# Kernel tuning notes

Measured on AMD Instinct MI355X. Metric: run time of the kernel, lower is better.

The kernel has to match this reference:

```python
import jax, jax.numpy as jnp
import numpy as np

N = 50000
E = 600000
D_IN = 128
D_HID = 128
D_OUT = 40
BN_EPS = 1e-5


def setup_inputs() -> dict:
    key = jax.random.key(0)
    ks = jax.random.split(key, 16)
    g = lambda k, *s: (jax.random.normal(k, s, jnp.float32) * 0.05)
    return {
        "x": jax.random.normal(ks[0], (N, D_IN), jnp.float32),
        "edge_index": jax.random.randint(ks[1], (2, E), 0, N, dtype=jnp.int64),
        "W0": g(ks[2], D_IN, D_HID), "b0": jnp.zeros((D_HID,), jnp.float32),
        "W1": g(ks[3], D_HID, D_HID), "b1": jnp.zeros((D_HID,), jnp.float32),
        "W2": g(ks[4], D_HID, D_OUT), "b2": jnp.zeros((D_OUT,), jnp.float32),
        "g0": 1.0 + g(ks[5], D_HID), "be0": g(ks[6], D_HID),
        "m0": g(ks[7], D_HID), "v0": 0.5 + jax.random.uniform(ks[8], (D_HID,), jnp.float32),
        "g1": 1.0 + g(ks[9], D_HID), "be1": g(ks[10], D_HID),
        "m1": g(ks[11], D_HID), "v1": 0.5 + jax.random.uniform(ks[12], (D_HID,), jnp.float32),
    }


def reference(x, edge_index, W0, b0, W1, b1, W2, b2,
              g0, be0, m0, v0, g1, be1, m1, v1):
    n = x.shape[0]
    loop = jnp.arange(n, dtype=edge_index.dtype)
    # GCN with self-loops: A_hat = A + I, symmetric normalization
    src = jnp.concatenate([edge_index[0], loop])
    dst = jnp.concatenate([edge_index[1], loop])
    deg = jax.ops.segment_sum(jnp.ones_like(dst, jnp.float32), dst, num_segments=n)
    dinv = jax.lax.rsqrt(jnp.maximum(deg, 1.0))
    norm = dinv[src] * dinv[dst]  # [E+N]

    def conv(h, W, b):
        h = h @ W + b                                   # [N, d_out]
        msg = norm[:, None] * h[src]                    # gather + scale
        return jax.ops.segment_sum(msg, dst, num_segments=n)

    def bn_relu(h, g, be, m, v):
        return jax.nn.relu((h - m) * (g * jax.lax.rsqrt(v + BN_EPS)) + be)

    h = bn_relu(conv(x, W0, b0), g0, be0, m0, v0)
    h = bn_relu(conv(h, W1, b1), g1, be1, m1, v1)
    h = conv(h, W2, b2)
    return jax.nn.log_softmax(h, axis=-1)
```

## Files before the change

kernel.cpp:

```cpp
#include <hip/hip_runtime.h>
#include <math.h>

#define BN_EPS 1e-5f
#define CAP 96

typedef unsigned short ushort_t;
typedef __attribute__((ext_vector_type(8))) short short8;
typedef __attribute__((ext_vector_type(4))) float floatx4;

__device__ inline ushort_t f2b(float f) {
    unsigned u = __float_as_uint(f);
    unsigned r = u + 0x7FFFu + ((u >> 16) & 1u);
    return (ushort_t)(r >> 16);
}
__device__ inline float b2f(ushort_t b) { return __uint_as_float(((unsigned)b) << 16); }
__device__ inline float2 u2f2(unsigned u) {
    return make_float2(b2f((ushort_t)(u & 0xffffu)), b2f((ushort_t)(u >> 16)));
}

__global__ __launch_bounds__(256) void fill_ell_cast(
    const int* __restrict__ ei, int* __restrict__ cnt, ushort_t* __restrict__ ell,
    const float* __restrict__ W0, const float* __restrict__ W1, const float* __restrict__ W2,
    ushort_t* __restrict__ Wt0, ushort_t* __restrict__ Wt1, ushort_t* __restrict__ Wt2,
    int E, int FB)
{
    int bid = blockIdx.x;
    if (bid < FB) {
        int e = bid * 256 + threadIdx.x;
        if (e < E) {
            int s = ei[e];
            int d = ei[E + e];
            int p = atomicAdd(&cnt[d], 1);
            if (p < CAP) ell[(size_t)d * CAP + p] = (ushort_t)s;
        }
        return;
    }
    int i = (bid - FB) * 256 + threadIdx.x;
    if (i < 16384) {
        int n = i >> 7, k = i & 127;
        Wt0[i] = f2b(W0[k * 128 + n]);
    } else if (i < 32768) {
        int j = i - 16384;
        int n = j >> 7, k = j & 127;
        Wt1[j] = f2b(W1[k * 128 + n]);
    } else if (i < 40960) {
        int j = i - 32768;
        int n = j >> 7, k = j & 127;
        Wt2[j] = (n < 40) ? f2b(W2[k * 40 + n]) : (ushort_t)0;
    }
}

__global__ void make_dinv(const int* __restrict__ cnt, float* __restrict__ dinv, int n) {
    int i = blockIdx.x * blockDim.x + threadIdx.x;
    if (i < n) dinv[i] = rsqrtf((float)(cnt[i] + 1));
}

template<int NT, bool AF32>
__global__ __launch_bounds__(256) void gemm_mfma(const void* __restrict__ Av,
                                                 const ushort_t* __restrict__ Wt,
                                                 const float* __restrict__ bias,
                                                 const float* __restrict__ dinv,
                                                 ushort_t* __restrict__ C,
                                                 int M, int ncols) {
    __shared__ ushort_t Ws[NT * 128];
    const int tid = threadIdx.x;
    const int rbase = blockIdx.x * 128;

#pragma unroll
    for (int p = 0; p < NT / 16; ++p) {
        int cid = p * 256 + tid;
        int nr = cid >> 4, seg = cid & 15;
        *(uint4*)(Ws + nr * 128 + ((seg ^ (nr & 15)) << 3)) =
            *(const uint4*)(Wt + (size_t)cid * 8);
    }
    __syncthreads();

    const int wave = tid >> 6, lane = tid & 63;
    const int m = lane & 15, quad = lane >> 4;
    constexpr int CT = NT / 16;
    floatx4 acc[2][CT];
#pragma unroll
    for (int rt = 0; rt < 2; ++rt)
#pragma unroll
        for (int ct = 0; ct < CT; ++ct) acc[rt][ct] = (floatx4){0.f, 0.f, 0.f, 0.f};

    const int r0 = wave * 32;
    const int ra = rbase + r0 + m;
    const int rb = ra + 16;
    const bool oka = ra < M, okb = rb < M;

#pragma unroll
    for (int ks = 0; ks < 4; ++ks) {
        int ko = ks * 32 + quad * 8;
        short8 a0 = {0, 0, 0, 0, 0, 0, 0, 0}, a1 = a0;
        if (AF32) {
            const float* A32 = (const float*)Av;
            if (oka) {
                const float* p = A32 + (size_t)ra * 128 + ko;
                float4 f0 = *(const float4*)p, f1 = *(const float4*)(p + 4);
                a0[0] = f2b(f0.x); a0[1] = f2b(f0.y); a0[2] = f2b(f0.z); a0[3] = f2b(f0.w);
                a0[4] = f2b(f1.x); a0[5] = f2b(f1.y); a0[6] = f2b(f1.z); a0[7] = f2b(f1.w);
            }
            if (okb) {
                const float* p = A32 + (size_t)rb * 128 + ko;
                float4 f0 = *(const float4*)p, f1 = *(const float4*)(p + 4);
                a1[0] = f2b(f0.x); a1[1] = f2b(f0.y); a1[2] = f2b(f0.z); a1[3] = f2b(f0.w);
                a1[4] = f2b(f1.x); a1[5] = f2b(f1.y); a1[6] = f2b(f1.z); a1[7] = f2b(f1.w);
            }
        } else {
            const ushort_t* A16 = (const ushort_t*)Av;
            if (oka) a0 = *(const short8*)(A16 + (size_t)ra * 128 + ko);
            if (okb) a1 = *(const short8*)(A16 + (size_t)rb * 128 + ko);
        }
#pragma unroll
        for (int ct = 0; ct < CT; ++ct) {
            short8 b = *(const short8*)(Ws + (ct * 16 + m) * 128 + (((ks * 4 + quad) ^ m) << 3));
            acc[0][ct] = __builtin_amdgcn_mfma_f32_16x16x32_bf16(a0, b, acc[0][ct], 0, 0, 0);
            acc[1][ct] = __builtin_amdgcn_mfma_f32_16x16x32_bf16(a1, b, acc[1][ct], 0, 0, 0);
        }
    }

    float dsc[2][4];
#pragma unroll
    for (int rt = 0; rt < 2; ++rt)
#pragma unroll
        for (int r = 0; r < 4; ++r) {
            int gr = rbase + r0 + rt * 16 + quad * 4 + r;
            dsc[rt][r] = (gr < M) ? dinv[gr] : 0.f;
        }

    __syncthreads();
    constexpr int SEGN = NT / 8, CMASK = SEGN - 1;
#pragma unroll
    for (int rt = 0; rt < 2; ++rt)
#pragma unroll
        for (int ct = 0; ct < CT; ++ct) {
            int col = ct * 16 + m;
            float bv = (col < ncols) ? bias[col] : 0.f;
            int seg = col >> 3, cl = col & 7;
#pragma unroll
            for (int r = 0; r < 4; ++r) {
                int row = r0 + rt * 16 + quad * 4 + r;
                Ws[row * NT + ((seg ^ (row & CMASK)) << 3) + cl] =
                    f2b((acc[rt][ct][r] + bv) * dsc[rt][r]);
            }
        }
    __syncthreads();
    constexpr int CPT = (128 * SEGN) / 256;
#pragma unroll
    for (int p = 0; p < CPT; ++p) {
        int cid = p * 256 + tid;
        int row = cid / SEGN, seg = cid & CMASK;
        int gr = rbase + row;
        if (gr < M)
            *(uint4*)(C + (size_t)gr * NT + seg * 8) =
                *(const uint4*)(Ws + row * NT + ((seg ^ (row & CMASK)) << 3));
    }
}

__global__ __launch_bounds__(256) void agg128_bn(const ushort_t* __restrict__ h,
                                                 const int* __restrict__ cnt,
                                                 const ushort_t* __restrict__ ell,
                                                 const float* __restrict__ dinv,
                                                 const float* __restrict__ g,
                                                 const float* __restrict__ be,
                                                 const float* __restrict__ mB,
                                                 const float* __restrict__ v,
                                                 ushort_t* __restrict__ out, int n) {
    int wv = __builtin_amdgcn_readfirstlane((blockIdx.x * 256 + threadIdx.x) >> 6);
    int lane = threadIdx.x & 63;
    if (wv >= n) return;
    const unsigned* h2 = (const unsigned*)h;
    float dv = dinv[wv];
    float2 hv = u2f2(h2[(size_t)wv * 64 + lane]);
    float ax = hv.x, ay = hv.y;
    int c = min(cnt[wv], CAP);
    const ushort_t* row = ell + (size_t)wv * CAP;
    int k = 0;
    for (; k + 8 <= c; k += 8) {
        int s[8];
#pragma unroll
        for (int j = 0; j < 8; ++j) s[j] = row[k + j];
#pragma unroll
        for (int j = 0; j < 8; ++j) {
            float2 t = u2f2(h2[(size_t)s[j] * 64 + lane]);
            ax += t.x;
            ay += t.y;
        }
    }
    if (k < c) {
        int rem = c - k;
        int s[8];
#pragma unroll
        for (int j = 0; j < 8; ++j) {
            int sr = row[k + j];
            s[j] = (j < rem) ? sr : 0;
        }
#pragma unroll
        for (int j = 0; j < 8; ++j) {
            float2 t = u2f2(h2[(size_t)s[j] * 64 + lane]);
            ax += (j < rem) ? t.x : 0.f;
            ay += (j < rem) ? t.y : 0.f;
        }
    }
    ax *= dv;
    ay *= dv;
    int c0 = lane * 2;
    float s0f = g[c0] * rsqrtf(v[c0] + BN_EPS);
    float s1f = g[c0 + 1] * rsqrtf(v[c0 + 1] + BN_EPS);
    float o0 = fmaxf(fmaf(ax - mB[c0], s0f, be[c0]), 0.f);
    float o1 = fmaxf(fmaf(ay - mB[c0 + 1], s1f, be[c0 + 1]), 0.f);
    unsigned ov = (unsigned)f2b(o0) | ((unsigned)f2b(o1) << 16);
    ((unsigned*)out)[(size_t)wv * 64 + lane] = ov;
}

__global__ __launch_bounds__(256) void agg40_lsm(const ushort_t* __restrict__ h,
                                                 const int* __restrict__ cnt,
                                                 const ushort_t* __restrict__ ell,
                                                 const float* __restrict__ dinv,
                                                 float* __restrict__ out, int n) {
    int wv = __builtin_amdgcn_readfirstlane((blockIdx.x * 256 + threadIdx.x) >> 6);
    int lane = threadIdx.x & 63;
    if (wv >= n) return;
    float dv = dinv[wv];
    float acc = b2f(h[(size_t)wv * 64 + lane]);
    int c = min(cnt[wv], CAP);
    const ushort_t* row = ell + (size_t)wv * CAP;
    int k = 0;
    for (; k + 8 <= c; k += 8) {
        int s[8];
#pragma unroll
        for (int j = 0; j < 8; ++j) s[j] = row[k + j];
#pragma unroll
        for (int j = 0; j < 8; ++j) acc += b2f(h[(size_t)s[j] * 64 + lane]);
    }
    if (k < c) {
        int rem = c - k;
        int s[8];
#pragma unroll
        for (int j = 0; j < 8; ++j) {
            int sr = row[k + j];
            s[j] = (j < rem) ? sr : 0;
        }
#pragma unroll
        for (int j = 0; j < 8; ++j) {
            float t = b2f(h[(size_t)s[j] * 64 + lane]);
            acc += (j < rem) ? t : 0.f;
        }
    }
    acc *= dv;
    bool act = lane < 40;
    float x = act ? acc : -INFINITY;
    float mx = x;
#pragma unroll
    for (int off = 32; off > 0; off >>= 1) mx = fmaxf(mx, __shfl_xor(mx, off, 64));
    float ex = act ? expf(acc - mx) : 0.f;
    float se = ex;
#pragma unroll
    for (int off = 32; off > 0; off >>= 1) se += __shfl_xor(se, off, 64);
    float r = acc - mx - logf(se);
    if (act) out[(size_t)wv * 40 + lane] = r;
}


extern "C" void kernel_launch(void* const* d_in, const int* in_sizes, int n_in,
                              void* d_out, int out_size, void* d_ws, size_t ws_size,
                              hipStream_t stream) {
    const float* x = (const float*)d_in[0];
    const int* ei = (const int*)d_in[1];
    const float* W0 = (const float*)d_in[2];
    const float* b0 = (const float*)d_in[3];
    const float* W1 = (const float*)d_in[4];
    const float* b1 = (const float*)d_in[5];
    const float* W2 = (const float*)d_in[6];
    const float* b2 = (const float*)d_in[7];
    const float* g0 = (const float*)d_in[8];
    const float* be0 = (const float*)d_in[9];
    const float* m0 = (const float*)d_in[10];
    const float* v0 = (const float*)d_in[11];
    const float* g1 = (const float*)d_in[12];
    const float* be1 = (const float*)d_in[13];
    const float* m1 = (const float*)d_in[14];
    const float* v1 = (const float*)d_in[15];
    float* out = (float*)d_out;

    const int N = in_sizes[0] / 128;
    const int E = in_sizes[1] / 2;

    char* wp = (char*)d_ws;
    auto alloc = [&](size_t bytes) -> char* {
        char* p = wp;
        wp += (bytes + 255) & ~(size_t)255;
        return p;
    };
    int* cnt = (int*)alloc((size_t)N * 4);
    float* dinv = (float*)alloc((size_t)N * 4);
    ushort_t* ell = (ushort_t*)alloc(((size_t)N * CAP + 16) * 2);
    ushort_t* hA = (ushort_t*)alloc((size_t)N * 128 * 2);
    ushort_t* hB = (ushort_t*)alloc((size_t)N * 128 * 2);
    ushort_t* hA2 = (ushort_t*)alloc((size_t)N * 128 * 2);
    ushort_t* hB2 = (ushort_t*)alloc((size_t)N * 128 * 2);
    ushort_t* hL = (ushort_t*)alloc((size_t)N * 64 * 2);
    ushort_t* Wt0 = (ushort_t*)alloc(128 * 128 * 2);
    ushort_t* Wt1 = (ushort_t*)alloc(128 * 128 * 2);
    ushort_t* Wt2 = (ushort_t*)alloc(64 * 128 * 2);

    const int GB = (N + 127) / 128;
    const int FB = (E + 255) / 256;
    const int CB = 160;

    hipMemsetAsync(cnt, 0, (size_t)N * 4, stream);
    fill_ell_cast<<<FB + CB, 256, 0, stream>>>(ei, cnt, ell, W0, W1, W2,
                                               Wt0, Wt1, Wt2, E, FB);
    make_dinv<<<(N + 255) / 256, 256, 0, stream>>>(cnt, dinv, N);

    gemm_mfma<128, true><<<GB, 256, 0, stream>>>(x, Wt0, b0, dinv, hA, N, 128);
    agg128_bn<<<(N + 3) / 4, 256, 0, stream>>>(hA, cnt, ell, dinv, g0, be0, m0, v0, hB, N);
    gemm_mfma<128, false><<<GB, 256, 0, stream>>>(hB, Wt1, b1, dinv, hA2, N, 128);
    agg128_bn<<<(N + 3) / 4, 256, 0, stream>>>(hA2, cnt, ell, dinv, g1, be1, m1, v1, hB2, N);
    gemm_mfma<64, false><<<GB, 256, 0, stream>>>(hB2, Wt2, b2, dinv, hL, N, 40);
    agg40_lsm<<<(N + 3) / 4, 256, 0, stream>>>(hL, cnt, ell, dinv, out, N);
}
```

Baseline: 231.8 us.

## Fuse all GCN stages into one cooperative persistent kernel with grid syncs

Replaces the sequence of eight launches (memset, fill, dinv, three GEMMs, three aggregations) with a single cooperative kernel. It runs persistent grid-stride loops over each phase and separates them with grid.sync. dinv is recomputed inline from the counts instead of being stored in its own buffer. This is meant to remove launch gaps and tail effects between stages, but it adds the cost of grid-wide barriers and limits each phase to a fixed resident grid, capped at 1024 blocks. The persistent GEMM also reloads the weights into LDS for every tile. A multi-kernel fallback path is kept in case the cooperative launch fails.

New measurement: 680.8 us. +193.7%, slower.

```diff
diff --git a/kernel.cpp b/kernel.cpp
--- a/kernel.cpp
+++ b/kernel.cpp
@@ -1,8 +1,12 @@
 #include <hip/hip_runtime.h>
+#include <hip/hip_cooperative_groups.h>
 #include <math.h>
+
+namespace cg = cooperative_groups;
 
 #define BN_EPS 1e-5f
 #define CAP 96
+#define GRID_MAX 1024
 
 typedef unsigned short ushort_t;
 typedef __attribute__((ext_vector_type(8))) short short8;
@@ -18,7 +22,291 @@
     return make_float2(b2f((ushort_t)(u & 0xffffu)), b2f((ushort_t)(u >> 16)));
 }
 
-__global__ __launch_bounds__(256) void fill_ell_cast(
+template<int NT, bool AF32>
+__device__ void gemm_phase(ushort_t* __restrict__ Ws,
+                           const void* __restrict__ Av,
+                           const ushort_t* __restrict__ Wt,
+                           const float* __restrict__ bias,
+                           const int* __restrict__ cnt,
+                           ushort_t* __restrict__ C,
+                           int M, int ncols) {
+    const int tid = threadIdx.x;
+    const int ntiles = (M + 127) >> 7;
+    const int wave = tid >> 6, lane = tid & 63;
+    const int m = lane & 15, quad = lane >> 4;
+    constexpr int CT = NT / 16;
+    const int r0 = wave * 32;
+
+    for (int t = blockIdx.x; t < ntiles; t += gridDim.x) {
+        const int rbase = t << 7;
+
+#pragma unroll
+        for (int p = 0; p < NT / 16; ++p) {
+            int cid = p * 256 + tid;
+            int nr = cid >> 4, seg = cid & 15;
+            *(uint4*)(Ws + nr * 128 + ((seg ^ (nr & 15)) << 3)) =
+                *(const uint4*)(Wt + (size_t)cid * 8);
+        }
+        __syncthreads();
+
+        floatx4 acc[2][CT];
+#pragma unroll
+        for (int rt = 0; rt < 2; ++rt)
+#pragma unroll
+            for (int ct = 0; ct < CT; ++ct) acc[rt][ct] = (floatx4){0.f, 0.f, 0.f, 0.f};
+
+        const int ra = rbase + r0 + m;
+        const int rb = ra + 16;
+        const bool oka = ra < M, okb = rb < M;
+
+#pragma unroll
+        for (int ks = 0; ks < 4; ++ks) {
+            int ko = ks * 32 + quad * 8;
+            short8 a0 = {0, 0, 0, 0, 0, 0, 0, 0}, a1 = a0;
+            if (AF32) {
+                const float* A32 = (const float*)Av;
+                if (oka) {
+                    const float* p = A32 + (size_t)ra * 128 + ko;
+                    float4 f0 = *(const float4*)p, f1 = *(const float4*)(p + 4);
+                    a0[0] = f2b(f0.x); a0[1] = f2b(f0.y); a0[2] = f2b(f0.z); a0[3] = f2b(f0.w);
+                    a0[4] = f2b(f1.x); a0[5] = f2b(f1.y); a0[6] = f2b(f1.z); a0[7] = f2b(f1.w);
+                }
+                if (okb) {
+                    const float* p = A32 + (size_t)rb * 128 + ko;
+                    float4 f0 = *(const float4*)p, f1 = *(const float4*)(p + 4);
+                    a1[0] = f2b(f0.x); a1[1] = f2b(f0.y); a1[2] = f2b(f0.z); a1[3] = f2b(f0.w);
+                    a1[4] = f2b(f1.x); a1[5] = f2b(f1.y); a1[6] = f2b(f1.z); a1[7] = f2b(f1.w);
+                }
+            } else {
+                const ushort_t* A16 = (const ushort_t*)Av;
+                if (oka) a0 = *(const short8*)(A16 + (size_t)ra * 128 + ko);
+                if (okb) a1 = *(const short8*)(A16 + (size_t)rb * 128 + ko);
+            }
+#pragma unroll
+            for (int ct = 0; ct < CT; ++ct) {
+                short8 b = *(const short8*)(Ws + (ct * 16 + m) * 128 + (((ks * 4 + quad) ^ m) << 3));
+                acc[0][ct] = __builtin_amdgcn_mfma_f32_16x16x32_bf16(a0, b, acc[0][ct], 0, 0, 0);
+                acc[1][ct] = __builtin_amdgcn_mfma_f32_16x16x32_bf16(a1, b, acc[1][ct], 0, 0, 0);
+            }
+        }
+
+        float dsc[2][4];
+#pragma unroll
+        for (int rt = 0; rt < 2; ++rt)
+#pragma unroll
+            for (int r = 0; r < 4; ++r) {
+                int gr = rbase + r0 + rt * 16 + quad * 4 + r;
+                dsc[rt][r] = (gr < M) ? rsqrtf((float)(cnt[gr] + 1)) : 0.f;
+            }
+
+        __syncthreads();
+        constexpr int SEGN = NT / 8, CMASK = SEGN - 1;
+#pragma unroll
+        for (int rt = 0; rt < 2; ++rt)
+#pragma unroll
+            for (int ct = 0; ct < CT; ++ct) {
+                int col = ct * 16 + m;
+                float bv = (col < ncols) ? bias[col] : 0.f;
+                int seg = col >> 3, cl = col & 7;
+#pragma unroll
+                for (int r = 0; r < 4; ++r) {
+                    int row = r0 + rt * 16 + quad * 4 + r;
+                    Ws[row * NT + ((seg ^ (row & CMASK)) << 3) + cl] =
+                        f2b((acc[rt][ct][r] + bv) * dsc[rt][r]);
+                }
+            }
+        __syncthreads();
+        constexpr int CPT = (128 * SEGN) / 256;
+#pragma unroll
+        for (int p = 0; p < CPT; ++p) {
+            int cid = p * 256 + tid;
+            int row = cid / SEGN, seg = cid & CMASK;
+            int gr = rbase + row;
+            if (gr < M)
+                *(uint4*)(C + (size_t)gr * NT + seg * 8) =
+                    *(const uint4*)(Ws + row * NT + ((seg ^ (row & CMASK)) << 3));
+        }
+        __syncthreads();
+    }
+}
+
+__device__ void agg128_phase(const ushort_t* __restrict__ h,
+                             const int* __restrict__ cnt,
+                             const ushort_t* __restrict__ ell,
+                             const float* __restrict__ g,
+                             const float* __restrict__ be,
+                             const float* __restrict__ mB,
+                             const float* __restrict__ v,
+                             ushort_t* __restrict__ out, int n) {
+    const int wslot = (blockIdx.x * 256 + threadIdx.x) >> 6;
+    const int lane = threadIdx.x & 63;
+    const int nw = gridDim.x * 4;
+    const unsigned* h2 = (const unsigned*)h;
+    const int c0 = lane * 2;
+    const float s0f = g[c0] * rsqrtf(v[c0] + BN_EPS);
+    const float s1f = g[c0 + 1] * rsqrtf(v[c0 + 1] + BN_EPS);
+    const float m0v = mB[c0], m1v = mB[c0 + 1], b0v = be[c0], b1v = be[c0 + 1];
+    for (int wv0 = wslot; wv0 < n; wv0 += nw) {
+        int wv = __builtin_amdgcn_readfirstlane(wv0);
+        int cd = cnt[wv];
+        float dv = rsqrtf((float)(cd + 1));
+        float2 hv = u2f2(h2[(size_t)wv * 64 + lane]);
+        float ax = hv.x, ay = hv.y;
+        int c = min(cd, CAP);
+        const ushort_t* row = ell + (size_t)wv * CAP;
+        int k = 0;
+        for (; k + 8 <= c; k += 8) {
+            int s[8];
+#pragma unroll
+            for (int j = 0; j < 8; ++j) s[j] = row[k + j];
+#pragma unroll
+            for (int j = 0; j < 8; ++j) {
+                float2 t = u2f2(h2[(size_t)s[j] * 64 + lane]);
+                ax += t.x;
+                ay += t.y;
+            }
+        }
+        if (k < c) {
+            int rem = c - k;
+            int s[8];
+#pragma unroll
+            for (int j = 0; j < 8; ++j) {
+                int sr = row[k + j];
+                s[j] = (j < rem) ? sr : 0;
+            }
+#pragma unroll
+            for (int j = 0; j < 8; ++j) {
+                float2 t = u2f2(h2[(size_t)s[j] * 64 + lane]);
+                ax += (j < rem) ? t.x : 0.f;
+                ay += (j < rem) ? t.y : 0.f;
+            }
+        }
+        ax *= dv;
+        ay *= dv;
+        float o0 = fmaxf(fmaf(ax - m0v, s0f, b0v), 0.f);
+        float o1 = fmaxf(fmaf(ay - m1v, s1f, b1v), 0.f);
+        unsigned ov = (unsigned)f2b(o0) | ((unsigned)f2b(o1) << 16);
+        ((unsigned*)out)[(size_t)wv * 64 + lane] = ov;
+    }
+}
+
+__device__ void agg40_phase(const ushort_t* __restrict__ h,
+                            const int* __restrict__ cnt,
+                            const ushort_t* __restrict__ ell,
+                            float* __restrict__ out, int n) {
+    const int wslot = (blockIdx.x * 256 + threadIdx.x) >> 6;
+    const int lane = threadIdx.x & 63;
+    const int nw = gridDim.x * 4;
+    for (int wv0 = wslot; wv0 < n; wv0 += nw) {
+        int wv = __builtin_amdgcn_readfirstlane(wv0);
+        int cd = cnt[wv];
+        float dv = rsqrtf((float)(cd + 1));
+        float acc = b2f(h[(size_t)wv * 64 + lane]);
+        int c = min(cd, CAP);
+        const ushort_t* row = ell + (size_t)wv * CAP;
+        int k = 0;
+        for (; k + 8 <= c; k += 8) {
+            int s[8];
+#pragma unroll
+            for (int j = 0; j < 8; ++j) s[j] = row[k + j];
+#pragma unroll
+            for (int j = 0; j < 8; ++j) acc += b2f(h[(size_t)s[j] * 64 + lane]);
+        }
+        if (k < c) {
+            int rem = c - k;
+            int s[8];
+#pragma unroll
+            for (int j = 0; j < 8; ++j) {
+                int sr = row[k + j];
+                s[j] = (j < rem) ? sr : 0;
+            }
+#pragma unroll
+            for (int j = 0; j < 8; ++j) {
+                float t = b2f(h[(size_t)s[j] * 64 + lane]);
+                acc += (j < rem) ? t : 0.f;
+            }
+        }
+        acc *= dv;
+        bool act = lane < 40;
+        float xv = act ? acc : -INFINITY;
+        float mx = xv;
+#pragma unroll
+        for (int off = 32; off > 0; off >>= 1) mx = fmaxf(mx, __shfl_xor(mx, off, 64));
+        float ex = act ? expf(acc - mx) : 0.f;
+        float se = ex;
+#pragma unroll
+        for (int off = 32; off > 0; off >>= 1) se += __shfl_xor(se, off, 64);
+        float r = acc - mx - logf(se);
+        if (act) out[(size_t)wv * 40 + lane] = r;
+    }
+}
+
+__device__ inline void cast_weights(const float* __restrict__ W0, const float* __restrict__ W1,
+                                    const float* __restrict__ W2, ushort_t* __restrict__ Wt0,
+                                    ushort_t* __restrict__ Wt1, ushort_t* __restrict__ Wt2,
+                                    int i) {
+    if (i < 16384) {
+        int nn = i >> 7, k = i & 127;
+        Wt0[i] = f2b(W0[k * 128 + nn]);
+    } else if (i < 32768) {
+        int j = i - 16384;
+        int nn = j >> 7, k = j & 127;
+        Wt1[j] = f2b(W1[k * 128 + nn]);
+    } else if (i < 40960) {
+        int j = i - 32768;
+        int nn = j >> 7, k = j & 127;
+        Wt2[j] = (nn < 40) ? f2b(W2[k * 40 + nn]) : (ushort_t)0;
+    }
+}
+
+__global__ __launch_bounds__(256, 4) void mega(
+    const float* __restrict__ x, const int* __restrict__ ei,
+    const float* __restrict__ W0, const float* __restrict__ b0,
+    const float* __restrict__ W1, const float* __restrict__ b1,
+    const float* __restrict__ W2, const float* __restrict__ b2,
+    const float* __restrict__ g0, const float* __restrict__ be0,
+    const float* __restrict__ m0, const float* __restrict__ v0,
+    const float* __restrict__ g1, const float* __restrict__ be1,
+    const float* __restrict__ m1, const float* __restrict__ v1,
+    float* __restrict__ out,
+    int* __restrict__ cnt, ushort_t* __restrict__ ell,
+    ushort_t* __restrict__ hA, ushort_t* __restrict__ hB,
+    ushort_t* __restrict__ hA2, ushort_t* __restrict__ hB2,
+    ushort_t* __restrict__ hL,
+    ushort_t* __restrict__ Wt0, ushort_t* __restrict__ Wt1, ushort_t* __restrict__ Wt2,
+    int N, int E)
+{
+    cg::grid_group grid = cg::this_grid();
+    __shared__ ushort_t Ws[128 * 128];
+    const int gtid = blockIdx.x * 256 + threadIdx.x;
+    const int gstr = gridDim.x * 256;
+
+    for (int i = gtid; i < N; i += gstr) cnt[i] = 0;
+    for (int i = gtid; i < 40960; i += gstr) cast_weights(W0, W1, W2, Wt0, Wt1, Wt2, i);
+    grid.sync();
+
+    for (int e = gtid; e < E; e += gstr) {
+        int s = ei[e];
+        int d = ei[E + e];
+        int p = atomicAdd(&cnt[d], 1);
+        if (p < CAP) ell[(size_t)d * CAP + p] = (ushort_t)s;
+    }
+    grid.sync();
+
+    gemm_phase<128, true>(Ws, x, Wt0, b0, cnt, hA, N, 128);
+    grid.sync();
+    agg128_phase(hA, cnt, ell, g0, be0, m0, v0, hB, N);
+    grid.sync();
+    gemm_phase<128, false>(Ws, hB, Wt1, b1, cnt, hA2, N, 128);
+    grid.sync();
+    agg128_phase(hA2, cnt, ell, g1, be1, m1, v1, hB2, N);
+    grid.sync();
+    gemm_phase<64, false>(Ws, hB2, Wt2, b2, cnt, hL, N, 40);
+    grid.sync();
+    agg40_phase(hL, cnt, ell, out, N);
+}
+
+__global__ __launch_bounds__(256) void k_fill_cast(
     const int* __restrict__ ei, int* __restrict__ cnt, ushort_t* __restrict__ ell,
     const float* __restrict__ W0, const float* __restrict__ W1, const float* __restrict__ W2,
     ushort_t* __restrict__ Wt0, ushort_t* __restrict__ Wt1, ushort_t* __restrict__ Wt2,
@@ -35,231 +323,35 @@
         }
         return;
     }
-    int i = (bid - FB) * 256 + threadIdx.x;
-    if (i < 16384) {
-        int n = i >> 7, k = i & 127;
-        Wt0[i] = f2b(W0[k * 128 + n]);
-    } else if (i < 32768) {
-        int j = i - 16384;
-        int n = j >> 7, k = j & 127;
-        Wt1[j] = f2b(W1[k * 128 + n]);
-    } else if (i < 40960) {
-        int j = i - 32768;
-        int n = j >> 7, k = j & 127;
-        Wt2[j] = (n < 40) ? f2b(W2[k * 40 + n]) : (ushort_t)0;
-    }
-}
-
-__global__ void make_dinv(const int* __restrict__ cnt, float* __restrict__ dinv, int n) {
-    int i = blockIdx.x * blockDim.x + threadIdx.x;
-    if (i < n) dinv[i] = rsqrtf((float)(cnt[i] + 1));
+    cast_weights(W0, W1, W2, Wt0, Wt1, Wt2, (bid - FB) * 256 + threadIdx.x);
 }
 
 template<int NT, bool AF32>
-__global__ __launch_bounds__(256) void gemm_mfma(const void* __restrict__ Av,
-                                                 const ushort_t* __restrict__ Wt,
-                                                 const float* __restrict__ bias,
-                                                 const float* __restrict__ dinv,
-                                                 ushort_t* __restrict__ C,
-                                                 int M, int ncols) {
+__global__ __launch_bounds__(256) void k_gemm(const void* __restrict__ Av,
+                                              const ushort_t* __restrict__ Wt,
+                                              const float* __restrict__ bias,
+                                              const int* __restrict__ cnt,
+                                              ushort_t* __restrict__ C, int M, int ncols) {
     __shared__ ushort_t Ws[NT * 128];
-    const int tid = threadIdx.x;
-    const int rbase = blockIdx.x * 128;
-
-#pragma unroll
-    for (int p = 0; p < NT / 16; ++p) {
-        int cid = p * 256 + tid;
-        int nr = cid >> 4, seg = cid & 15;
-        *(uint4*)(Ws + nr * 128 + ((seg ^ (nr & 15)) << 3)) =
-            *(const uint4*)(Wt + (size_t)cid * 8);
-    }
-    __syncthreads();
-
-    const int wave = tid >> 6, lane = tid & 63;
-    const int m = lane & 15, quad = lane >> 4;
-    constexpr int CT = NT / 16;
-    floatx4 acc[2][CT];
-#pragma unroll
-    for (int rt = 0; rt < 2; ++rt)
-#pragma unroll
-        for (int ct = 0; ct < CT; ++ct) acc[rt][ct] = (floatx4){0.f, 0.f, 0.f, 0.f};
-
-    const int r0 = wave * 32;
-    const int ra = rbase + r0 + m;
-    const int rb = ra + 16;
-    const bool oka = ra < M, okb = rb < M;
-
-#pragma unroll
-    for (int ks = 0; ks < 4; ++ks) {
-        int ko = ks * 32 + quad * 8;
-        short8 a0 = {0, 0, 0, 0, 0, 0, 0, 0}, a1 = a0;
-        if (AF32) {
-            const float* A32 = (const float*)Av;
-            if (oka) {
-                const float* p = A32 + (size_t)ra * 128 + ko;
-                float4 f0 = *(const float4*)p, f1 = *(const float4*)(p + 4);
-                a0[0] = f2b(f0.x); a0[1] = f2b(f0.y); a0[2] = f2b(f0.z); a0[3] = f2b(f0.w);
-                a0[4] = f2b(f1.x); a0[5] = f2b(f1.y); a0[6] = f2b(f1.z); a0[7] = f2b(f1.w);
-            }
-            if (okb) {
-                const float* p = A32 + (size_t)rb * 128 + ko;
-                float4 f0 = *(const float4*)p, f1 = *(const float4*)(p + 4);
-                a1[0] = f2b(f0.x); a1[1] = f2b(f0.y); a1[2] = f2b(f0.z); a1[3] = f2b(f0.w);
-                a1[4] = f2b(f1.x); a1[5] = f2b(f1.y); a1[6] = f2b(f1.z); a1[7] = f2b(f1.w);
-            }
-        } else {
-            const ushort_t* A16 = (const ushort_t*)Av;
-            if (oka) a0 = *(const short8*)(A16 + (size_t)ra * 128 + ko);
-            if (okb) a1 = *(const short8*)(A16 + (size_t)rb * 128 + ko);
-        }
-#pragma unroll
-        for (int ct = 0; ct < CT; ++ct) {
-            short8 b = *(const short8*)(Ws + (ct * 16 + m) * 128 + (((ks * 4 + quad) ^ m) << 3));
-            acc[0][ct] = __builtin_amdgcn_mfma_f32_16x16x32_bf16(a0, b, acc[0][ct], 0, 0, 0);
-            acc[1][ct] = __builtin_amdgcn_mfma_f32_16x16x32_bf16(a1, b, acc[1][ct], 0, 0, 0);
-        }
-    }
-
-    float dsc[2][4];
-#pragma unroll
-    for (int rt = 0; rt < 2; ++rt)
-#pragma unroll
-        for (int r = 0; r < 4; ++r) {
-            int gr = rbase + r0 + rt * 16 + quad * 4 + r;
-            dsc[rt][r] = (gr < M) ? dinv[gr] : 0.f;
-        }
-
-    __syncthreads();
-    constexpr int SEGN = NT / 8, CMASK = SEGN - 1;
-#pragma unroll
-    for (int rt = 0; rt < 2; ++rt)
-#pragma unroll
-        for (int ct = 0; ct < CT; ++ct) {
-            int col = ct * 16 + m;
-            float bv = (col < ncols) ? bias[col] : 0.f;
-            int seg = col >> 3, cl = col & 7;
-#pragma unroll
-            for (int r = 0; r < 4; ++r) {
-                int row = r0 + rt * 16 + quad * 4 + r;
-                Ws[row * NT + ((seg ^ (row & CMASK)) << 3) + cl] =
-                    f2b((acc[rt][ct][r] + bv) * dsc[rt][r]);
-            }
-        }
-    __syncthreads();
-    constexpr int CPT = (128 * SEGN) / 256;
-#pragma unroll
-    for (int p = 0; p < CPT; ++p) {
-        int cid = p * 256 + tid;
-        int row = cid / SEGN, seg = cid & CMASK;
-        int gr = rbase + row;
-        if (gr < M)
-            *(uint4*)(C + (size_t)gr * NT + seg * 8) =
-                *(const uint4*)(Ws + row * NT + ((seg ^ (row & CMASK)) << 3));
-    }
-}
-
-__global__ __launch_bounds__(256) void agg128_bn(const ushort_t* __restrict__ h,
-                                                 const int* __restrict__ cnt,
-                                                 const ushort_t* __restrict__ ell,
-                                                 const float* __restrict__ dinv,
-                                                 const float* __restrict__ g,
-                                                 const float* __restrict__ be,
-                                                 const float* __restrict__ mB,
-                                                 const float* __restrict__ v,
-                                                 ushort_t* __restrict__ out, int n) {
-    int wv = __builtin_amdgcn_readfirstlane((blockIdx.x * 256 + threadIdx.x) >> 6);
-    int lane = threadIdx.x & 63;
-    if (wv >= n) return;
-    const unsigned* h2 = (const unsigned*)h;
-    float dv = dinv[wv];
-    float2 hv = u2f2(h2[(size_t)wv * 64 + lane]);
-    float ax = hv.x, ay = hv.y;
-    int c = min(cnt[wv], CAP);
-    const ushort_t* row = ell + (size_t)wv * CAP;
-    int k = 0;
-    for (; k + 8 <= c; k += 8) {
-        int s[8];
-#pragma unroll
-        for (int j = 0; j < 8; ++j) s[j] = row[k + j];
-#pragma unroll
-        for (int j = 0; j < 8; ++j) {
-            float2 t = u2f2(h2[(size_t)s[j] * 64 + lane]);
-            ax += t.x;
-            ay += t.y;
-        }
-    }
-    if (k < c) {
-        int rem = c - k;
-        int s[8];
-#pragma unroll
-        for (int j = 0; j < 8; ++j) {
-            int sr = row[k + j];
-            s[j] = (j < rem) ? sr : 0;
-        }
-#pragma unroll
-        for (int j = 0; j < 8; ++j) {
-            float2 t = u2f2(h2[(size_t)s[j] * 64 + lane]);
-            ax += (j < rem) ? t.x : 0.f;
-            ay += (j < rem) ? t.y : 0.f;
-        }
-    }
-    ax *= dv;
-    ay *= dv;
-    int c0 = lane * 2;
-    float s0f = g[c0] * rsqrtf(v[c0] + BN_EPS);
-    float s1f = g[c0 + 1] * rsqrtf(v[c0 + 1] + BN_EPS);
-    float o0 = fmaxf(fmaf(ax - mB[c0], s0f, be[c0]), 0.f);
-    float o1 = fmaxf(fmaf(ay - mB[c0 + 1], s1f, be[c0 + 1]), 0.f);
-    unsigned ov = (unsigned)f2b(o0) | ((unsigned)f2b(o1) << 16);
-    ((unsigned*)out)[(size_t)wv * 64 + lane] = ov;
-}
-
-__global__ __launch_bounds__(256) void agg40_lsm(const ushort_t* __restrict__ h,
-                                                 const int* __restrict__ cnt,
-                                                 const ushort_t* __restrict__ ell,
-                                                 const float* __restrict__ dinv,
-                                                 float* __restrict__ out, int n) {
-    int wv = __builtin_amdgcn_readfirstlane((blockIdx.x * 256 + threadIdx.x) >> 6);
-    int lane = threadIdx.x & 63;
-    if (wv >= n) return;
-    float dv = dinv[wv];
-    float acc = b2f(h[(size_t)wv * 64 + lane]);
-    int c = min(cnt[wv], CAP);
-    const ushort_t* row = ell + (size_t)wv * CAP;
-    int k = 0;
-    for (; k + 8 <= c; k += 8) {
-        int s[8];
-#pragma unroll
-        for (int j = 0; j < 8; ++j) s[j] = row[k + j];
-#pragma unroll
-        for (int j = 0; j < 8; ++j) acc += b2f(h[(size_t)s[j] * 64 + lane]);
-    }
-    if (k < c) {
-        int rem = c - k;
-        int s[8];
-#pragma unroll
-        for (int j = 0; j < 8; ++j) {
-            int sr = row[k + j];
-            s[j] = (j < rem) ? sr : 0;
-        }
-#pragma unroll
-        for (int j = 0; j < 8; ++j) {
-            float t = b2f(h[(size_t)s[j] * 64 + lane]);
-            acc += (j < rem) ? t : 0.f;
-        }
-    }
-    acc *= dv;
-    bool act = lane < 40;
-    float x = act ? acc : -INFINITY;
-    float mx = x;
-#pragma unroll
-    for (int off = 32; off > 0; off >>= 1) mx = fmaxf(mx, __shfl_xor(mx, off, 64));
-    float ex = act ? expf(acc - mx) : 0.f;
-    float se = ex;
-#pragma unroll
-    for (int off = 32; off > 0; off >>= 1) se += __shfl_xor(se, off, 64);
-    float r = acc - mx - logf(se);
-    if (act) out[(size_t)wv * 40 + lane] = r;
+    gemm_phase<NT, AF32>(Ws, Av, Wt, bias, cnt, C, M, ncols);
+}
+
+__global__ __launch_bounds__(256) void k_agg128(const ushort_t* __restrict__ h,
+                                                const int* __restrict__ cnt,
+                                                const ushort_t* __restrict__ ell,
+                                                const float* __restrict__ g,
+                                                const float* __restrict__ be,
+                                                const float* __restrict__ mB,
+                                                const float* __restrict__ v,
+                                                ushort_t* __restrict__ out, int n) {
+    agg128_phase(h, cnt, ell, g, be, mB, v, out, n);
+}
+
+__global__ __launch_bounds__(256) void k_agg40(const ushort_t* __restrict__ h,
+                                               const int* __restrict__ cnt,
+                                               const ushort_t* __restrict__ ell,
+                                               float* __restrict__ out, int n) {
+    agg40_phase(h, cnt, ell, out, n);
 }
 
 
@@ -284,8 +376,8 @@
     const float* v1 = (const float*)d_in[15];
     float* out = (float*)d_out;
 
-    const int N = in_sizes[0] / 128;
-    const int E = in_sizes[1] / 2;
+    int N = in_sizes[0] / 128;
+    int E = in_sizes[1] / 2;
 
     char* wp = (char*)d_ws;
     auto alloc = [&](size_t bytes) -> char* {
@@ -294,7 +386,6 @@
         return p;
     };
     int* cnt = (int*)alloc((size_t)N * 4);
-    float* dinv = (float*)alloc((size_t)N * 4);
     ushort_t* ell = (ushort_t*)alloc(((size_t)N * CAP + 16) * 2);
     ushort_t* hA = (ushort_t*)alloc((size_t)N * 128 * 2);
     ushort_t* hB = (ushort_t*)alloc((size_t)N * 128 * 2);
@@ -305,19 +396,38 @@
     ushort_t* Wt1 = (ushort_t*)alloc(128 * 128 * 2);
     ushort_t* Wt2 = (ushort_t*)alloc(64 * 128 * 2);
 
-    const int GB = (N + 127) / 128;
-    const int FB = (E + 255) / 256;
-    const int CB = 160;
-
-    hipMemsetAsync(cnt, 0, (size_t)N * 4, stream);
-    fill_ell_cast<<<FB + CB, 256, 0, stream>>>(ei, cnt, ell, W0, W1, W2,
-                                               Wt0, Wt1, Wt2, E, FB);
-    make_dinv<<<(N + 255) / 256, 256, 0, stream>>>(cnt, dinv, N);
-
-    gemm_mfma<128, true><<<GB, 256, 0, stream>>>(x, Wt0, b0, dinv, hA, N, 128);
-    agg128_bn<<<(N + 3) / 4, 256, 0, stream>>>(hA, cnt, ell, dinv, g0, be0, m0, v0, hB, N);
-    gemm_mfma<128, false><<<GB, 256, 0, stream>>>(hB, Wt1, b1, dinv, hA2, N, 128);
-    agg128_bn<<<(N + 3) / 4, 256, 0, stream>>>(hA2, cnt, ell, dinv, g1, be1, m1, v1, hB2, N);
-    gemm_mfma<64, false><<<GB, 256, 0, stream>>>(hB2, Wt2, b2, dinv, hL, N, 40);
-    agg40_lsm<<<(N + 3) / 4, 256, 0, stream>>>(hL, cnt, ell, dinv, out, N);
-}
+    static int coop_grid = -1;
+    if (coop_grid < 0) {
+        int dev = 0, ncu = 0, bpc = 0;
+        hipGetDevice(&dev);
+        hipDeviceGetAttribute(&ncu, hipDeviceAttributeMultiprocessorCount, dev);
+        if (hipOccupancyMaxActiveBlocksPerMultiprocessor(&bpc, (const void*)mega, 256, 0)
+                != hipSuccess || bpc < 1)
+            bpc = 1;
+        long g = (long)ncu * bpc;
+        coop_grid = (int)(g < GRID_MAX ? g : GRID_MAX);
+        if (coop_grid < 1) coop_grid = 1;
+    }
+
+    void* args[] = {&x,  &ei,  &W0,  &b0,  &W1,  &b1,  &W2,  &b2,
+                    &g0, &be0, &m0,  &v0,  &g1,  &be1, &m1,  &v1,
+                    &out, &cnt, &ell, &hA, &hB, &hA2, &hB2, &hL,
+                    &Wt0, &Wt1, &Wt2, &N, &E};
+    hipError_t err = hipLaunchCooperativeKernel((void*)mega, dim3(coop_grid), dim3(256),
+                                                args, 0, stream);
+    if (err != hipSuccess) {
+        (void)hipGetLastError();
+        const int GB = (N + 127) / 128;
+        const int FB = (E + 255) / 256;
+        const int CB = 160;
+        hipMemsetAsync(cnt, 0, (size_t)N * 4, stream);
+        k_fill_cast<<<FB + CB, 256, 0, stream>>>(ei, cnt, ell, W0, W1, W2,
+                                                 Wt0, Wt1, Wt2, E, FB);
+        k_gemm<128, true><<<GB, 256, 0, stream>>>(x, Wt0, b0, cnt, hA, N, 128);
+        k_agg128<<<(N + 3) / 4, 256, 0, stream>>>(hA, cnt, ell, g0, be0, m0, v0, hB, N);
+        k_gemm<128, false><<<GB, 256, 0, stream>>>(hB, Wt1, b1, cnt, hA2, N, 128);
+        k_agg128<<<(N + 3) / 4, 256, 0, stream>>>(hA2, cnt, ell, g1, be1, m1, v1, hB2, N);
+        k_gemm<64, false><<<GB, 256, 0, stream>>>(hB2, Wt2, b2, cnt, hL, N, 40);
+        k_agg40<<<(N + 3) / 4, 256, 0, stream>>>(hL, cnt, ell, out, N);
+    }
+}
```
